# Performance work log

Hardware: AMD Instinct MI355X
Metric: run time of the kernel (lower is better)

## Reference

```python
import jax, jax.numpy as jnp
import numpy as np

EMBED = 128
HEADS = 32
HEAD_DIM = EMBED // HEADS  # 4
BATCH = 32
SEQ = 2048


def setup_inputs() -> dict:
    key = jax.random.key(0)
    ks = jax.random.split(key, 6)
    s = 1.0 / np.sqrt(EMBED)
    return {
        "x": jax.random.normal(ks[0], (BATCH, SEQ, EMBED), dtype=jnp.float32),
        # torch Linear weights are (out_features, in_features)
        "Wq": jax.random.uniform(ks[1], (EMBED, EMBED), jnp.float32, -s, s),
        "Wk": jax.random.uniform(ks[2], (EMBED, EMBED), jnp.float32, -s, s),
        "Wv": jax.random.uniform(ks[3], (EMBED, EMBED), jnp.float32, -s, s),
        "Wo": jax.random.uniform(ks[4], (EMBED, EMBED), jnp.float32, -s, s),
        "bo": jax.random.uniform(ks[5], (EMBED,), jnp.float32, -s, s),
    }


def reference(x, Wq, Wk, Wv, Wo, bo):
    b, s, e = x.shape
    h, d = HEADS, HEAD_DIM
    # projections (torch Linear: x @ W.T)
    q = (x @ Wq.T).reshape(b, s, h, d)
    k = (x @ Wk.T).reshape(b, s, h, d)
    v = (x @ Wv.T).reshape(b, s, h, d)
    # FAITHFUL to source: einsum 'bnqh,bnkh->bnqk' on (b, seq, heads, head_dim)
    # => n = seq position, q/k = HEADS. Attention is over the heads axis.
    scale = 1.0 / (float(d) ** 0.5)
    scores = jnp.einsum('bnqh,bnkh->bnqk', q, k) * scale  # (b, seq, heads, heads)
    attn = jax.nn.softmax(scores, axis=-1)
    attended = jnp.einsum('bnqk,bnkv->bnqv', attn, v).reshape(b, s, e)
    return attended @ Wo.T + bo
```

## Files before the change

kernel.cpp:

```cpp
#include <hip/hip_runtime.h>


#define TOKENS (32 * 2048)
#define E 128
#define NH 32
#define BT 16
#define THREADS 128
#define LPITCH 136

typedef __attribute__((ext_vector_type(8))) short short8;
typedef __attribute__((ext_vector_type(4))) float f32x4;
typedef __attribute__((ext_vector_type(16))) float f32x16;
typedef __fp16 h2_t __attribute__((ext_vector_type(2)));
typedef __fp16 h8_t __attribute__((ext_vector_type(8)));

#if __has_builtin(__builtin_amdgcn_exp2f)
#define EXP2F __builtin_amdgcn_exp2f
#else
#define EXP2F exp2f
#endif

#if __has_builtin(__builtin_amdgcn_rcpf)
#define RCPF __builtin_amdgcn_rcpf
#else
#define RCPF(x) (1.0f / (x))
#endif

static __device__ __forceinline__ unsigned short f2bf(float f) {
    unsigned u = __float_as_uint(f);
    unsigned r = (u + 0x7fffu + ((u >> 16) & 1u)) >> 16;
    return (unsigned short)r;
}

static __device__ __forceinline__ unsigned pk16(float a, float b) {
    return __builtin_bit_cast(unsigned, __builtin_amdgcn_cvt_pkrtz(a, b));
}

static __device__ __forceinline__ f32x16 zero16() {
    f32x16 z;
#pragma unroll
    for (int i = 0; i < 16; ++i) z[i] = 0.f;
    return z;
}

static __device__ __forceinline__ int vperm(int kh) {
    return ((kh >> 4) & 1) * 16 + ((kh >> 2) & 1) * 8 + ((kh >> 3) & 1) * 4 + (kh & 3);
}

__global__ void pack_w(const float* __restrict__ Wq, const float* __restrict__ Wk,
                       const float* __restrict__ Wv, const float* __restrict__ Wo,
                       unsigned short* __restrict__ wpk) {
    int idx = blockIdx.x * blockDim.x + threadIdx.x;
    if (idx >= 4 * 8 * 4 * 64) return;
    int lane = idx & 63;
    int ks   = (idx >> 6) & 3;
    int nt   = (idx >> 8) & 7;
    int proj = idx >> 11;
    const float* W = (proj == 0) ? Wq : (proj == 1) ? Wk : (proj == 2) ? Wv : Wo;
    int c = lane & 15, g = lane >> 4;
    const float* src = W + (size_t)(nt * 16 + c) * E + ks * 32 + g * 8;
    unsigned short* dst = wpk + (size_t)idx * 8;
    if (proj < 3) {
#pragma unroll
        for (int j = 0; j < 8; ++j) dst[j] = f2bf(src[j]);
    } else {
#pragma unroll
        for (int j = 0; j < 8; ++j)
            dst[j] = __builtin_bit_cast(unsigned short, (__fp16)src[j]);
    }
}

__global__ __launch_bounds__(THREADS) void mha_fused(
        const float* __restrict__ x, const unsigned short* __restrict__ wpk,
        const float* __restrict__ bo, float* __restrict__ out) {
    __shared__ __fp16 qs [BT * LPITCH];
    __shared__ __fp16 ksh[BT * LPITCH];
    __shared__ __fp16 vth[BT * LPITCH];
    __shared__ __fp16 at_[BT * LPITCH];

    const int tid  = threadIdx.x;
    const int wave = tid >> 6;
    const int lane = tid & 63;
    const int c = lane & 15, g = lane >> 4;
    const int bt0 = blockIdx.x * BT;

    {
        short8 afrag[4];
        const float* xrow = x + (size_t)(bt0 + c) * E;
#pragma unroll
        for (int ks2 = 0; ks2 < 4; ++ks2) {
            const float* p = xrow + ks2 * 32 + g * 8;
            float4 v0 = *(const float4*)(p);
            float4 v1 = *(const float4*)(p + 4);
            short8 a;
            a[0] = f2bf(v0.x); a[1] = f2bf(v0.y); a[2] = f2bf(v0.z); a[3] = f2bf(v0.w);
            a[4] = f2bf(v1.x); a[5] = f2bf(v1.y); a[6] = f2bf(v1.z); a[7] = f2bf(v1.w);
            afrag[ks2] = a;
        }

#pragma unroll
        for (int i = 0; i < 12; ++i) {
            int nc   = wave * 12 + i;
            int proj = nc >> 3;
            int nt   = nc & 7;
            const unsigned short* wb = wpk + ((size_t)((proj * 8 + nt) * 4) * 64 + lane) * 8;
            f32x4 acc = {0.f, 0.f, 0.f, 0.f};
#pragma unroll
            for (int ks2 = 0; ks2 < 4; ++ks2) {
                short8 b = *(const short8*)(wb + (size_t)ks2 * 64 * 8);
                acc = __builtin_amdgcn_mfma_f32_16x16x32_bf16(afrag[ks2], b, acc, 0, 0, 0);
            }
            int col = nt * 16 + c;
            if (proj < 2) {
                __fp16* dst = proj ? ksh : qs;
#pragma unroll
                for (int r2 = 0; r2 < 4; ++r2) {
                    int row = g * 4 + r2;
                    dst[row * LPITCH + col] = (__fp16)acc[r2];
                }
            } else {
                int vc = (col & 3) * 32 + vperm(col >> 2);
#pragma unroll
                for (int r2 = 0; r2 < 4; ++r2) {
                    int row = g * 4 + r2;
                    vth[row * LPITCH + vc] = (__fp16)acc[r2];
                }
            }
        }
    }
    __syncthreads();

    {
        const float cexp = 0.5f * 1.44269504088896340736f;
        const int c32 = lane & 31;
        const int gg  = lane >> 5;
        const uint4 ONES4 = make_uint4(0x3C003C00u, 0x3C003C00u, 0x3C003C00u, 0x3C003C00u);
#pragma unroll 2
        for (int t8 = 0; t8 < 8; ++t8) {
            const int tok = wave * 8 + t8;
            const __fp16* qrow = qs  + tok * LPITCH;
            const __fp16* krow = ksh + tok * LPITCH;
            const __fp16* vrow = vth + tok * LPITCH;

            uint4 kraw = {0u, 0u, 0u, 0u}, qraw = {0u, 0u, 0u, 0u};
            if (gg == 0) {
                uint2 kk = *(const uint2*)(krow + c32 * 4);
                uint2 qq = *(const uint2*)(qrow + c32 * 4);
                kraw.x = kk.x; kraw.y = kk.y;
                qraw.x = qq.x; qraw.y = qq.y;
            }
            h8_t kf = __builtin_bit_cast(h8_t, kraw);
            h8_t qf = __builtin_bit_cast(h8_t, qraw);

            f32x16 sc = zero16();
            sc = __builtin_amdgcn_mfma_f32_32x32x16_f16(kf, qf, sc, 0, 0, 0);

            float e[16];
#pragma unroll
            for (int r = 0; r < 16; ++r) e[r] = EXP2F(sc[r] * cexp);
            uint4 p0u = make_uint4(pk16(e[0], e[1]),  pk16(e[2], e[3]),
                                   pk16(e[4], e[5]),  pk16(e[6], e[7]));
            uint4 p1u = make_uint4(pk16(e[8], e[9]),  pk16(e[10], e[11]),
                                   pk16(e[12], e[13]), pk16(e[14], e[15]));
            h8_t p0 = __builtin_bit_cast(h8_t, p0u);
            h8_t p1 = __builtin_bit_cast(h8_t, p1u);

            uint4 vr0 = *(const uint4*)(vrow + (c32 & 3) * 32 + gg * 8);
            uint4 vr1 = *(const uint4*)(vrow + (c32 & 3) * 32 + 16 + gg * 8);
            if (c32 == 4) { vr0 = ONES4; vr1 = ONES4; }
            h8_t v0f = __builtin_bit_cast(h8_t, vr0);
            h8_t v1f = __builtin_bit_cast(h8_t, vr1);

            f32x16 pv = zero16();
            pv = __builtin_amdgcn_mfma_f32_32x32x16_f16(v0f, p0, pv, 0, 0, 0);
            pv = __builtin_amdgcn_mfma_f32_32x32x16_f16(v1f, p1, pv, 0, 0, 0);

            float sum  = __shfl(pv[0], c32 + 32, 64);
            float rinv = RCPF(sum);
            if (lane < 32) {
                unsigned short h0 = __builtin_bit_cast(unsigned short, (__fp16)(pv[0] * rinv));
                unsigned short h1 = __builtin_bit_cast(unsigned short, (__fp16)(pv[1] * rinv));
                unsigned short h2 = __builtin_bit_cast(unsigned short, (__fp16)(pv[2] * rinv));
                unsigned short h3 = __builtin_bit_cast(unsigned short, (__fp16)(pv[3] * rinv));
                uint2 st;
                st.x = (unsigned)h0 | ((unsigned)h1 << 16);
                st.y = (unsigned)h2 | ((unsigned)h3 << 16);
                *(uint2*)(at_ + tok * LPITCH + c32 * 4) = st;
            }
        }
    }
    __syncthreads();

    {
        h8_t af[4];
#pragma unroll
        for (int ks2 = 0; ks2 < 4; ++ks2) {
            af[ks2] = *(const h8_t*)(at_ + c * LPITCH + ks2 * 32 + g * 8);
        }
#pragma unroll
        for (int i = 0; i < 4; ++i) {
            int nt = wave * 4 + i;
            const unsigned short* wb = wpk + ((size_t)((3 * 8 + nt) * 4) * 64 + lane) * 8;
            f32x4 acc = {0.f, 0.f, 0.f, 0.f};
#pragma unroll
            for (int ks2 = 0; ks2 < 4; ++ks2) {
                h8_t b = *(const h8_t*)(wb + (size_t)ks2 * 64 * 8);
                acc = __builtin_amdgcn_mfma_f32_16x16x32_f16(af[ks2], b, acc, 0, 0, 0);
            }
            int col = nt * 16 + c;
            float bias = bo[col];
            float* orow = out + (size_t)(bt0 + g * 4) * E + col;
#pragma unroll
            for (int r2 = 0; r2 < 4; ++r2) {
                orow[(size_t)r2 * E] = acc[r2] + bias;
            }
        }
    }
}

extern "C" void kernel_launch(void* const* d_in, const int* in_sizes, int n_in,
                              void* d_out, int out_size, void* d_ws, size_t ws_size,
                              hipStream_t stream) {
    const float* x  = (const float*)d_in[0];
    const float* Wq = (const float*)d_in[1];
    const float* Wk = (const float*)d_in[2];
    const float* Wv = (const float*)d_in[3];
    const float* Wo = (const float*)d_in[4];
    const float* bo = (const float*)d_in[5];
    unsigned short* wpk = (unsigned short*)d_ws;
    float* out = (float*)d_out;

    pack_w<<<32, 256, 0, stream>>>(Wq, Wk, Wv, Wo, wpk);
    mha_fused<<<TOKENS / BT, THREADS, 0, stream>>>(x, wpk, bo, out);
}
```

Measured before the change: 46.08 us.

## Switch to fp16 projections, transpose MFMA operands, vectorize stores, pair attention tokens

Converts x and all weights to fp16 with hardware packed conversion instead of manual bf16 rounding, and folds the softmax scale and log2e into the packed Wk weights. It swaps MFMA operand order so each lane holds contiguous output columns, which allows vectorized LDS stores and float4 global output stores with a float4 bias load. The attention loop now handles two tokens per iteration for more MFMA/exp overlap, and the attention output reuses the q buffer to cut LDS use. Risks include fp16 range or precision loss on x and the projections, and extra register pressure from the paired tokens.

```diff
diff --git a/kernel.cpp b/kernel.cpp
--- a/kernel.cpp
+++ b/kernel.cpp
@@ -8,10 +8,8 @@
 #define THREADS 128
 #define LPITCH 136
 
-typedef __attribute__((ext_vector_type(8))) short short8;
 typedef __attribute__((ext_vector_type(4))) float f32x4;
 typedef __attribute__((ext_vector_type(16))) float f32x16;
-typedef __fp16 h2_t __attribute__((ext_vector_type(2)));
 typedef __fp16 h8_t __attribute__((ext_vector_type(8)));
 
 #if __has_builtin(__builtin_amdgcn_exp2f)
@@ -26,12 +24,6 @@
 #define RCPF(x) (1.0f / (x))
 #endif
 
-static __device__ __forceinline__ unsigned short f2bf(float f) {
-    unsigned u = __float_as_uint(f);
-    unsigned r = (u + 0x7fffu + ((u >> 16) & 1u)) >> 16;
-    return (unsigned short)r;
-}
-
 static __device__ __forceinline__ unsigned pk16(float a, float b) {
     return __builtin_bit_cast(unsigned, __builtin_amdgcn_cvt_pkrtz(a, b));
 }
@@ -49,7 +41,7 @@
 
 __global__ void pack_w(const float* __restrict__ Wq, const float* __restrict__ Wk,
                        const float* __restrict__ Wv, const float* __restrict__ Wo,
-                       unsigned short* __restrict__ wpk) {
+                       __fp16* __restrict__ wpk) {
     int idx = blockIdx.x * blockDim.x + threadIdx.x;
     if (idx >= 4 * 8 * 4 * 64) return;
     int lane = idx & 63;
@@ -57,26 +49,20 @@
     int nt   = (idx >> 8) & 7;
     int proj = idx >> 11;
     const float* W = (proj == 0) ? Wq : (proj == 1) ? Wk : (proj == 2) ? Wv : Wo;
+    float scl = (proj == 1) ? 0.72134752044448170f : 1.0f;
     int c = lane & 15, g = lane >> 4;
     const float* src = W + (size_t)(nt * 16 + c) * E + ks * 32 + g * 8;
-    unsigned short* dst = wpk + (size_t)idx * 8;
-    if (proj < 3) {
-#pragma unroll
-        for (int j = 0; j < 8; ++j) dst[j] = f2bf(src[j]);
-    } else {
-#pragma unroll
-        for (int j = 0; j < 8; ++j)
-            dst[j] = __builtin_bit_cast(unsigned short, (__fp16)src[j]);
-    }
+    __fp16* dst = wpk + (size_t)idx * 8;
+#pragma unroll
+    for (int j = 0; j < 8; ++j) dst[j] = (__fp16)(src[j] * scl);
 }
 
 __global__ __launch_bounds__(THREADS) void mha_fused(
-        const float* __restrict__ x, const unsigned short* __restrict__ wpk,
+        const float* __restrict__ x, const __fp16* __restrict__ wpk,
         const float* __restrict__ bo, float* __restrict__ out) {
-    __shared__ __fp16 qs [BT * LPITCH];
-    __shared__ __fp16 ksh[BT * LPITCH];
-    __shared__ __fp16 vth[BT * LPITCH];
-    __shared__ __fp16 at_[BT * LPITCH];
+    __shared__ __align__(16) __fp16 qs [BT * LPITCH];
+    __shared__ __align__(16) __fp16 ksh[BT * LPITCH];
+    __shared__ __align__(16) __fp16 vth[BT * LPITCH];
 
     const int tid  = threadIdx.x;
     const int wave = tid >> 6;
@@ -85,107 +71,118 @@
     const int bt0 = blockIdx.x * BT;
 
     {
-        short8 afrag[4];
+        h8_t afrag[4];
         const float* xrow = x + (size_t)(bt0 + c) * E;
 #pragma unroll
         for (int ks2 = 0; ks2 < 4; ++ks2) {
             const float* p = xrow + ks2 * 32 + g * 8;
             float4 v0 = *(const float4*)(p);
             float4 v1 = *(const float4*)(p + 4);
-            short8 a;
-            a[0] = f2bf(v0.x); a[1] = f2bf(v0.y); a[2] = f2bf(v0.z); a[3] = f2bf(v0.w);
-            a[4] = f2bf(v1.x); a[5] = f2bf(v1.y); a[6] = f2bf(v1.z); a[7] = f2bf(v1.w);
-            afrag[ks2] = a;
+            uint4 au;
+            au.x = pk16(v0.x, v0.y);
+            au.y = pk16(v0.z, v0.w);
+            au.z = pk16(v1.x, v1.y);
+            au.w = pk16(v1.z, v1.w);
+            afrag[ks2] = __builtin_bit_cast(h8_t, au);
         }
 
 #pragma unroll
         for (int i = 0; i < 12; ++i) {
-            int nc   = wave * 12 + i;
-            int proj = nc >> 3;
+            int nc   = i * 2 + wave;
+            int proj = i >> 2;
             int nt   = nc & 7;
-            const unsigned short* wb = wpk + ((size_t)((proj * 8 + nt) * 4) * 64 + lane) * 8;
+            const __fp16* wb = wpk + ((size_t)((proj * 8 + nt) * 4) * 64 + lane) * 8;
             f32x4 acc = {0.f, 0.f, 0.f, 0.f};
 #pragma unroll
             for (int ks2 = 0; ks2 < 4; ++ks2) {
-                short8 b = *(const short8*)(wb + (size_t)ks2 * 64 * 8);
-                acc = __builtin_amdgcn_mfma_f32_16x16x32_bf16(afrag[ks2], b, acc, 0, 0, 0);
-            }
-            int col = nt * 16 + c;
+                h8_t wf = *(const h8_t*)(wb + (size_t)ks2 * 64 * 8);
+                acc = __builtin_amdgcn_mfma_f32_16x16x32_f16(wf, afrag[ks2], acc, 0, 0, 0);
+            }
             if (proj < 2) {
                 __fp16* dst = proj ? ksh : qs;
-#pragma unroll
-                for (int r2 = 0; r2 < 4; ++r2) {
-                    int row = g * 4 + r2;
-                    dst[row * LPITCH + col] = (__fp16)acc[r2];
-                }
+                uint2 st = make_uint2(pk16(acc[0], acc[1]), pk16(acc[2], acc[3]));
+                *(uint2*)(dst + c * LPITCH + nt * 16 + g * 4) = st;
             } else {
-                int vc = (col & 3) * 32 + vperm(col >> 2);
-#pragma unroll
-                for (int r2 = 0; r2 < 4; ++r2) {
-                    int row = g * 4 + r2;
-                    vth[row * LPITCH + vc] = (__fp16)acc[r2];
-                }
+                int vp = vperm(nt * 4 + g);
+#pragma unroll
+                for (int r2 = 0; r2 < 4; ++r2)
+                    vth[c * LPITCH + r2 * 32 + vp] = (__fp16)acc[r2];
             }
         }
     }
     __syncthreads();
 
     {
-        const float cexp = 0.5f * 1.44269504088896340736f;
         const int c32 = lane & 31;
         const int gg  = lane >> 5;
         const uint4 ONES4 = make_uint4(0x3C003C00u, 0x3C003C00u, 0x3C003C00u, 0x3C003C00u);
-#pragma unroll 2
-        for (int t8 = 0; t8 < 8; ++t8) {
-            const int tok = wave * 8 + t8;
-            const __fp16* qrow = qs  + tok * LPITCH;
-            const __fp16* krow = ksh + tok * LPITCH;
-            const __fp16* vrow = vth + tok * LPITCH;
-
-            uint4 kraw = {0u, 0u, 0u, 0u}, qraw = {0u, 0u, 0u, 0u};
+        const f32x16 z = zero16();
+        const int tb = wave * 8;
+#pragma unroll 1
+        for (int pr = 0; pr < 4; ++pr) {
+            const int t0 = tb + pr * 2, t1 = t0 + 1;
+            const __fp16* v0r = vth + t0 * LPITCH;
+            const __fp16* v1r = vth + t1 * LPITCH;
+
+            uint4 ka0 = {0u,0u,0u,0u}, qa0 = {0u,0u,0u,0u};
+            uint4 ka1 = {0u,0u,0u,0u}, qa1 = {0u,0u,0u,0u};
             if (gg == 0) {
-                uint2 kk = *(const uint2*)(krow + c32 * 4);
-                uint2 qq = *(const uint2*)(qrow + c32 * 4);
-                kraw.x = kk.x; kraw.y = kk.y;
-                qraw.x = qq.x; qraw.y = qq.y;
-            }
-            h8_t kf = __builtin_bit_cast(h8_t, kraw);
-            h8_t qf = __builtin_bit_cast(h8_t, qraw);
-
-            f32x16 sc = zero16();
-            sc = __builtin_amdgcn_mfma_f32_32x32x16_f16(kf, qf, sc, 0, 0, 0);
-
-            float e[16];
-#pragma unroll
-            for (int r = 0; r < 16; ++r) e[r] = EXP2F(sc[r] * cexp);
-            uint4 p0u = make_uint4(pk16(e[0], e[1]),  pk16(e[2], e[3]),
-                                   pk16(e[4], e[5]),  pk16(e[6], e[7]));
-            uint4 p1u = make_uint4(pk16(e[8], e[9]),  pk16(e[10], e[11]),
-                                   pk16(e[12], e[13]), pk16(e[14], e[15]));
-            h8_t p0 = __builtin_bit_cast(h8_t, p0u);
-            h8_t p1 = __builtin_bit_cast(h8_t, p1u);
-
-            uint4 vr0 = *(const uint4*)(vrow + (c32 & 3) * 32 + gg * 8);
-            uint4 vr1 = *(const uint4*)(vrow + (c32 & 3) * 32 + 16 + gg * 8);
-            if (c32 == 4) { vr0 = ONES4; vr1 = ONES4; }
-            h8_t v0f = __builtin_bit_cast(h8_t, vr0);
-            h8_t v1f = __builtin_bit_cast(h8_t, vr1);
-
-            f32x16 pv = zero16();
-            pv = __builtin_amdgcn_mfma_f32_32x32x16_f16(v0f, p0, pv, 0, 0, 0);
-            pv = __builtin_amdgcn_mfma_f32_32x32x16_f16(v1f, p1, pv, 0, 0, 0);
-
-            float sum  = __shfl(pv[0], c32 + 32, 64);
-            float rinv = RCPF(sum);
+                uint2 t;
+                t = *(const uint2*)(ksh + t0 * LPITCH + c32 * 4); ka0.x = t.x; ka0.y = t.y;
+                t = *(const uint2*)(qs  + t0 * LPITCH + c32 * 4); qa0.x = t.x; qa0.y = t.y;
+                t = *(const uint2*)(ksh + t1 * LPITCH + c32 * 4); ka1.x = t.x; ka1.y = t.y;
+                t = *(const uint2*)(qs  + t1 * LPITCH + c32 * 4); qa1.x = t.x; qa1.y = t.y;
+            }
+            uint4 va00 = *(const uint4*)(v0r + (c32 & 3) * 32 + gg * 8);
+            uint4 va01 = *(const uint4*)(v0r + (c32 & 3) * 32 + 16 + gg * 8);
+            uint4 va10 = *(const uint4*)(v1r + (c32 & 3) * 32 + gg * 8);
+            uint4 va11 = *(const uint4*)(v1r + (c32 & 3) * 32 + 16 + gg * 8);
+            if (c32 == 4) { va00 = ONES4; va01 = ONES4; va10 = ONES4; va11 = ONES4; }
+
+            f32x16 sc0 = __builtin_amdgcn_mfma_f32_32x32x16_f16(
+                __builtin_bit_cast(h8_t, ka0), __builtin_bit_cast(h8_t, qa0), z, 0, 0, 0);
+            f32x16 sc1 = __builtin_amdgcn_mfma_f32_32x32x16_f16(
+                __builtin_bit_cast(h8_t, ka1), __builtin_bit_cast(h8_t, qa1), z, 0, 0, 0);
+
+            uint4 p00u, p01u, p10u, p11u;
+            {
+                float e[16];
+#pragma unroll
+                for (int r = 0; r < 16; ++r) e[r] = EXP2F(sc0[r]);
+                p00u = make_uint4(pk16(e[0], e[1]),  pk16(e[2], e[3]),
+                                  pk16(e[4], e[5]),  pk16(e[6], e[7]));
+                p01u = make_uint4(pk16(e[8], e[9]),  pk16(e[10], e[11]),
+                                  pk16(e[12], e[13]), pk16(e[14], e[15]));
+            }
+            {
+                float e[16];
+#pragma unroll
+                for (int r = 0; r < 16; ++r) e[r] = EXP2F(sc1[r]);
+                p10u = make_uint4(pk16(e[0], e[1]),  pk16(e[2], e[3]),
+                                  pk16(e[4], e[5]),  pk16(e[6], e[7]));
+                p11u = make_uint4(pk16(e[8], e[9]),  pk16(e[10], e[11]),
+                                  pk16(e[12], e[13]), pk16(e[14], e[15]));
+            }
+
+            f32x16 pv0 = __builtin_amdgcn_mfma_f32_32x32x16_f16(
+                __builtin_bit_cast(h8_t, va00), __builtin_bit_cast(h8_t, p00u), z, 0, 0, 0);
+            pv0 = __builtin_amdgcn_mfma_f32_32x32x16_f16(
+                __builtin_bit_cast(h8_t, va01), __builtin_bit_cast(h8_t, p01u), pv0, 0, 0, 0);
+            f32x16 pv1 = __builtin_amdgcn_mfma_f32_32x32x16_f16(
+                __builtin_bit_cast(h8_t, va10), __builtin_bit_cast(h8_t, p10u), z, 0, 0, 0);
+            pv1 = __builtin_amdgcn_mfma_f32_32x32x16_f16(
+                __builtin_bit_cast(h8_t, va11), __builtin_bit_cast(h8_t, p11u), pv1, 0, 0, 0);
+
+            float s0 = __shfl(pv0[0], c32 + 32, 64);
+            float s1 = __shfl(pv1[0], c32 + 32, 64);
+            float r0 = RCPF(s0), r1 = RCPF(s1);
             if (lane < 32) {
-                unsigned short h0 = __builtin_bit_cast(unsigned short, (__fp16)(pv[0] * rinv));
-                unsigned short h1 = __builtin_bit_cast(unsigned short, (__fp16)(pv[1] * rinv));
-                unsigned short h2 = __builtin_bit_cast(unsigned short, (__fp16)(pv[2] * rinv));
-                unsigned short h3 = __builtin_bit_cast(unsigned short, (__fp16)(pv[3] * rinv));
-                uint2 st;
-                st.x = (unsigned)h0 | ((unsigned)h1 << 16);
-                st.y = (unsigned)h2 | ((unsigned)h3 << 16);
-                *(uint2*)(at_ + tok * LPITCH + c32 * 4) = st;
+                uint2 st0 = make_uint2(pk16(pv0[0] * r0, pv0[1] * r0),
+                                       pk16(pv0[2] * r0, pv0[3] * r0));
+                uint2 st1 = make_uint2(pk16(pv1[0] * r1, pv1[1] * r1),
+                                       pk16(pv1[2] * r1, pv1[3] * r1));
+                *(uint2*)(qs + t0 * LPITCH + c32 * 4) = st0;
+                *(uint2*)(qs + t1 * LPITCH + c32 * 4) = st1;
             }
         }
     }
@@ -195,25 +192,23 @@
         h8_t af[4];
 #pragma unroll
         for (int ks2 = 0; ks2 < 4; ++ks2) {
-            af[ks2] = *(const h8_t*)(at_ + c * LPITCH + ks2 * 32 + g * 8);
+            af[ks2] = *(const h8_t*)(qs + c * LPITCH + ks2 * 32 + g * 8);
         }
 #pragma unroll
         for (int i = 0; i < 4; ++i) {
             int nt = wave * 4 + i;
-            const unsigned short* wb = wpk + ((size_t)((3 * 8 + nt) * 4) * 64 + lane) * 8;
+            const __fp16* wb = wpk + ((size_t)((3 * 8 + nt) * 4) * 64 + lane) * 8;
             f32x4 acc = {0.f, 0.f, 0.f, 0.f};
 #pragma unroll
             for (int ks2 = 0; ks2 < 4; ++ks2) {
                 h8_t b = *(const h8_t*)(wb + (size_t)ks2 * 64 * 8);
-                acc = __builtin_amdgcn_mfma_f32_16x16x32_f16(af[ks2], b, acc, 0, 0, 0);
-            }
-            int col = nt * 16 + c;
-            float bias = bo[col];
-            float* orow = out + (size_t)(bt0 + g * 4) * E + col;
-#pragma unroll
-            for (int r2 = 0; r2 < 4; ++r2) {
-                orow[(size_t)r2 * E] = acc[r2] + bias;
-            }
+                acc = __builtin_amdgcn_mfma_f32_16x16x32_f16(b, af[ks2], acc, 0, 0, 0);
+            }
+            int col0 = nt * 16 + g * 4;
+            float4 b4 = *(const float4*)(bo + col0);
+            float4 st = make_float4(acc[0] + b4.x, acc[1] + b4.y,
+                                    acc[2] + b4.z, acc[3] + b4.w);
+            *(float4*)(out + (size_t)(bt0 + c) * E + col0) = st;
         }
     }
 }
@@ -227,7 +222,7 @@
     const float* Wv = (const float*)d_in[3];
     const float* Wo = (const float*)d_in[4];
     const float* bo = (const float*)d_in[5];
-    unsigned short* wpk = (unsigned short*)d_ws;
+    __fp16* wpk = (__fp16*)d_ws;
     float* out = (float*)d_out;
 
     pack_w<<<32, 256, 0, stream>>>(Wq, Wk, Wv, Wo, wpk);
```

After: 46.09 us. Within noise of the previous version (+0.0%).
